# Optimization experiments

Measured on AMD Instinct MI355X. Metric: run time of the kernel, lower is better.

## Reference

```python
import jax, jax.numpy as jnp
import numpy as np

HEAD_DIM = 256
L2_EPS = 1e-12  # tf.math.l2_normalize default epsilon


def setup_inputs() -> dict:
    key = jax.random.key(0)
    ks = jax.random.split(key, 6)
    B, U = 64, 2048
    D_dec, D_enc = 1024, 512
    H, K, A = 4, HEAD_DIM, 1024
    s = 0.075  # RandomUniform(-0.075, 0.075) kernel init
    return {
        "dec_state": jax.random.normal(ks[0], (B, D_dec), jnp.float32),
        "enc_state": jax.random.normal(ks[1], (B, U, D_enc), jnp.float32),
        "phi_w": jax.random.uniform(ks[2], (H, D_dec, K), jnp.float32, -s, s),
        "phi_b": jnp.zeros((H, K), jnp.float32),
        "psi_w": jax.random.uniform(ks[3], (H, D_enc, K), jnp.float32, -s, s),
        "psi_b": jnp.zeros((H, K), jnp.float32),
        "out_w": jax.random.uniform(ks[4], (H * D_enc, A), jnp.float32, -s, s),
        "out_b": jnp.zeros((A,), jnp.float32),
    }


def reference(dec_state, enc_state, phi_w, phi_b, psi_w, psi_b, out_w, out_b):
    B = dec_state.shape[0]
    # Per-head query/key projections, all heads at once.
    phi_s = jnp.einsum("bd,hdk->bhk", dec_state, phi_w) + phi_b[None]      # (B,H,K)
    psi_h = jnp.einsum("bue,hek->bhuk", enc_state, psi_w) + psi_b[None, :, None]  # (B,H,U,K)
    scale = 1.0 / jnp.sqrt(jnp.asarray(HEAD_DIM, jnp.float32))
    energy = jnp.einsum("bhk,bhuk->bhu", phi_s, psi_h) * scale              # (B,H,U)
    attn = jax.nn.softmax(energy, axis=-1)
    # NOTE: the original attends over the RAW enc_state (not psi_h).
    ctx = jnp.einsum("bhu,bue->bhe", attn, enc_state)                        # (B,H,E)
    # tf.math.l2_normalize over last axis
    sq = jnp.sum(ctx * ctx, axis=-1, keepdims=True)
    ctx = ctx * jax.lax.rsqrt(jnp.maximum(sq, L2_EPS))
    combined = ctx.reshape(B, -1)                                            # (B, H*E) == concat over heads
    return combined @ out_w + out_b
```

## Files before the change

kernel.cpp:

```cpp
#include <hip/hip_runtime.h>
#include <math.h>

typedef float f2 __attribute__((ext_vector_type(2)));

constexpr int NB = 64;
constexpr int NU = 2048;
constexpr int ND = 1024;
constexpr int NE = 512;
constexpr int NH = 4;
constexpr int NK = 256;
constexpr int NA = 1024;
constexpr int NS = 16;
constexpr int ROWS_PER_BLOCK = NU / NS;
constexpr int ROWS_PER_WAVE  = ROWS_PER_BLOCK / 4;
constexpr float SCALE = 0.0625f;

constexpr int RSPLIT = 16;
constexpr int RCH = (NH*NE)/RSPLIT;
constexpr int BT = 8;

constexpr size_t WS_Q   = 0;
constexpr size_t WS_CTX = WS_Q + (size_t)NB*NH*NE;

__global__ __launch_bounds__(1024) void k_phi_q(
    const float* __restrict__ dec, const float* __restrict__ phi_w,
    const float* __restrict__ phi_b, const float* __restrict__ psi_w,
    float* __restrict__ q, float* __restrict__ ctxacc,
    const float* __restrict__ out_b, float* __restrict__ out)
{
  const int bi = blockIdx.x;
  const int b = bi >> 2;
  const int h = bi & 3;
  const int t = threadIdx.x;
  if (t < 512) ctxacc[(size_t)bi*512 + t] = 0.f;
  if (t < 256) out[(size_t)bi*256 + t] = out_b[(bi*256 + t) & (NA-1)];

  __shared__ float dec_lds[ND];
  __shared__ float par[4][NK];
  __shared__ float phi_lds[NK];
  dec_lds[t] = dec[(size_t)b*ND + t];
  __syncthreads();
  const int k  = t & 255;
  const int dq = t >> 8;
  const float* pw = phi_w + (size_t)h*ND*NK + (size_t)(dq*256)*NK + k;
  float s = 0.f;
  #pragma unroll 16
  for (int d = 0; d < 256; ++d) s += dec_lds[dq*256 + d] * pw[(size_t)d*NK];
  par[dq][k] = s;
  __syncthreads();
  if (t < NK)
    phi_lds[t] = par[0][t] + par[1][t] + par[2][t] + par[3][t] + phi_b[h*NK + t];
  __syncthreads();
  if (t < NE) {
    const float4* row = (const float4*)(psi_w + ((size_t)h*NE + t)*NK);
    float acc = 0.f;
    #pragma unroll 16
    for (int kk = 0; kk < NK/4; ++kk) {
      float4 v = row[kk];
      float4 p = ((const float4*)phi_lds)[kk];
      acc += v.x*p.x + v.y*p.y + v.z*p.z + v.w*p.w;
    }
    q[((size_t)b*NH + h)*NE + t] = acc;
  }
}

__global__ __launch_bounds__(256, 4) void k_flash(
    const float* __restrict__ enc, const float* __restrict__ qg,
    float* __restrict__ ctxacc)
{
  const int s = blockIdx.x;
  const int b = blockIdx.y;
  const int t = threadIdx.x;
  const int wave = t >> 6;
  const int lane = t & 63;

  f2 qv[NH][4];
  const float* qb = qg + (size_t)b*NH*NE;
  #pragma unroll
  for (int h = 0; h < NH; ++h) {
    float4 a0 = *(const float4*)(qb + h*NE + 4*lane);
    float4 a1 = *(const float4*)(qb + h*NE + 256 + 4*lane);
    qv[h][0] = f2{a0.x, a0.y}; qv[h][1] = f2{a0.z, a0.w};
    qv[h][2] = f2{a1.x, a1.y}; qv[h][3] = f2{a1.z, a1.w};
  }
  f2 acc2[NH][4];
  #pragma unroll
  for (int h = 0; h < NH; ++h)
    #pragma unroll
    for (int j = 0; j < 4; ++j) acc2[h][j] = f2{0.f, 0.f};

  const int u0 = s*ROWS_PER_BLOCK + wave*ROWS_PER_WAVE;
  const float* encb = enc + ((size_t)b*NU + u0)*NE;
  #pragma unroll 2
  for (int r = 0; r < ROWS_PER_WAVE; ++r) {
    float4 v0 = *(const float4*)(encb + (size_t)r*NE + 4*lane);
    float4 v1 = *(const float4*)(encb + (size_t)r*NE + 256 + 4*lane);
    f2 e0 = f2{v0.x, v0.y}, e1 = f2{v0.z, v0.w};
    f2 e2 = f2{v1.x, v1.y}, e3 = f2{v1.z, v1.w};
    float d[NH];
    #pragma unroll
    for (int h = 0; h < NH; ++h) {
      f2 p = e0*qv[h][0] + e1*qv[h][1] + e2*qv[h][2] + e3*qv[h][3];
      d[h] = p[0] + p[1];
    }
    #pragma unroll
    for (int off = 1; off < 64; off <<= 1) {
      #pragma unroll
      for (int h = 0; h < NH; ++h) d[h] += __shfl_xor(d[h], off);
    }
    #pragma unroll
    for (int h = 0; h < NH; ++h) {
      float pf = __expf(d[h] * SCALE);
      f2 pp = f2{pf, pf};
      acc2[h][0] += pp*e0; acc2[h][1] += pp*e1;
      acc2[h][2] += pp*e2; acc2[h][3] += pp*e3;
    }
  }
  __shared__ float acc_lds[4][NH][NE];
  #pragma unroll
  for (int h = 0; h < NH; ++h) {
    *(float4*)&acc_lds[wave][h][4*lane] =
        make_float4(acc2[h][0][0], acc2[h][0][1], acc2[h][1][0], acc2[h][1][1]);
    *(float4*)&acc_lds[wave][h][256 + 4*lane] =
        make_float4(acc2[h][2][0], acc2[h][2][1], acc2[h][3][0], acc2[h][3][1]);
  }
  __syncthreads();
  float* cb = ctxacc + (size_t)b*(NH*NE);
  #pragma unroll
  for (int h = 0; h < NH; ++h) {
    #pragma unroll
    for (int eo = 0; eo < 2; ++eo) {
      int e = t + eo*256;
      float v = acc_lds[0][h][e] + acc_lds[1][h][e] + acc_lds[2][h][e] + acc_lds[3][h][e];
      unsafeAtomicAdd(&cb[h*NE + e], v);
    }
  }
}

__global__ __launch_bounds__(256) void k_out(
    const float* __restrict__ ctxacc, const float* __restrict__ out_w,
    float* __restrict__ out)
{
  const int t = threadIdx.x;
  const int a = blockIdx.x*256 + t;
  const int b0 = blockIdx.y * BT;
  const int rc = blockIdx.z;
  const int h  = rc >> 2;
  const int e0 = (rc & 3) * RCH;

  __shared__ float rn_lds[BT];
  const int wv = t >> 6, lane = t & 63;
  {
    const int i = 2*wv + (lane >> 5);
    const int l32 = lane & 31;
    const float* row = ctxacc + (size_t)(b0+i)*(NH*NE) + (size_t)h*NE;
    float ss = 0.f;
    #pragma unroll
    for (int j = 0; j < 16; ++j) { float v = row[l32 + 32*j]; ss += v*v; }
    #pragma unroll
    for (int off = 1; off < 32; off <<= 1) ss += __shfl_xor(ss, off);
    if (l32 == 0) rn_lds[i] = rsqrtf(fmaxf(ss, 1e-12f));
  }
  __syncthreads();

  __shared__ float c_lds[RCH][BT];
  for (int g = t; g < RCH*BT; g += 256) {
    const int r = g & (RCH-1), i = g >> 7;
    c_lds[r][i] = ctxacc[(size_t)(b0+i)*(NH*NE) + (size_t)h*NE + e0 + r] * rn_lds[i];
  }
  __syncthreads();

  float accv[BT];
  #pragma unroll
  for (int i = 0; i < BT; ++i) accv[i] = 0.f;
  const float* w = out_w + ((size_t)rc*RCH)*NA + a;
  #pragma unroll 8
  for (int r = 0; r < RCH; ++r) {
    float wvv = w[(size_t)r*NA];
    float4 ca = *(const float4*)&c_lds[r][0];
    float4 cb = *(const float4*)&c_lds[r][4];
    accv[0] += ca.x*wvv; accv[1] += ca.y*wvv; accv[2] += ca.z*wvv; accv[3] += ca.w*wvv;
    accv[4] += cb.x*wvv; accv[5] += cb.y*wvv; accv[6] += cb.z*wvv; accv[7] += cb.w*wvv;
  }
  #pragma unroll
  for (int i = 0; i < BT; ++i)
    unsafeAtomicAdd(&out[(size_t)(b0+i)*NA + a], accv[i]);
}

extern "C" void kernel_launch(void* const* d_in, const int* in_sizes, int n_in,
                              void* d_out, int out_size, void* d_ws, size_t ws_size,
                              hipStream_t stream) {
  const float* dec   = (const float*)d_in[0];
  const float* enc   = (const float*)d_in[1];
  const float* phi_w = (const float*)d_in[2];
  const float* phi_b = (const float*)d_in[3];
  const float* psi_w = (const float*)d_in[4];
  const float* out_w = (const float*)d_in[6];
  const float* out_b = (const float*)d_in[7];
  float* out = (float*)d_out;
  float* ws = (float*)d_ws;
  float* q      = ws + WS_Q;
  float* ctxacc = ws + WS_CTX;

  hipLaunchKernelGGL(k_phi_q, dim3(NB*NH),                 dim3(1024), 0, stream,
                     dec, phi_w, phi_b, psi_w, q, ctxacc, out_b, out);
  hipLaunchKernelGGL(k_flash, dim3(NS, NB),                dim3(256),  0, stream,
                     enc, q, ctxacc);
  hipLaunchKernelGGL(k_out,   dim3(NA/256, NB/BT, RSPLIT), dim3(256),  0, stream,
                     ctxacc, out_w, out);
}
```

Before: 94.69 us.

## Split query projection into batched tiled GEMM kernels with split-K partials

Replaces the per-(batch, head) query projection kernel with two tiled GEMM kernels. Each weight element of phi_w and psi_w is now reused across 16 batch rows in registers, instead of being reread once per batch. The first kernel writes split-D partial sums to a new workspace buffer. The second reduces those partials, adds the bias, multiplies by a psi_w tile held in LDS, and accumulates q with atomics. This is meant to cut redundant weight traffic in the prologue, at the cost of an extra launch, a partial-sum buffer and atomic adds.

```diff
diff --git a/kernel.cpp b/kernel.cpp
--- a/kernel.cpp
+++ b/kernel.cpp
@@ -19,49 +19,114 @@
 constexpr int RCH = (NH*NE)/RSPLIT;
 constexpr int BT = 8;
 
+constexpr int DSP = 16;
+constexpr int KSP = 4;
+
 constexpr size_t WS_Q   = 0;
 constexpr size_t WS_CTX = WS_Q + (size_t)NB*NH*NE;
-
-__global__ __launch_bounds__(1024) void k_phi_q(
+constexpr size_t WS_P   = WS_CTX + (size_t)NB*NH*NE;
+
+__global__ __launch_bounds__(256) void k_phi(
     const float* __restrict__ dec, const float* __restrict__ phi_w,
-    const float* __restrict__ phi_b, const float* __restrict__ psi_w,
-    float* __restrict__ q, float* __restrict__ ctxacc,
+    float* __restrict__ P, float* __restrict__ q, float* __restrict__ ctxacc,
     const float* __restrict__ out_b, float* __restrict__ out)
 {
-  const int bi = blockIdx.x;
-  const int b = bi >> 2;
-  const int h = bi & 3;
-  const int t = threadIdx.x;
-  if (t < 512) ctxacc[(size_t)bi*512 + t] = 0.f;
-  if (t < 256) out[(size_t)bi*256 + t] = out_b[(bi*256 + t) & (NA-1)];
-
-  __shared__ float dec_lds[ND];
-  __shared__ float par[4][NK];
-  __shared__ float phi_lds[NK];
-  dec_lds[t] = dec[(size_t)b*ND + t];
-  __syncthreads();
-  const int k  = t & 255;
-  const int dq = t >> 8;
-  const float* pw = phi_w + (size_t)h*ND*NK + (size_t)(dq*256)*NK + k;
-  float s = 0.f;
-  #pragma unroll 16
-  for (int d = 0; d < 256; ++d) s += dec_lds[dq*256 + d] * pw[(size_t)d*NK];
-  par[dq][k] = s;
-  __syncthreads();
-  if (t < NK)
-    phi_lds[t] = par[0][t] + par[1][t] + par[2][t] + par[3][t] + phi_b[h*NK + t];
-  __syncthreads();
-  if (t < NE) {
-    const float4* row = (const float4*)(psi_w + ((size_t)h*NE + t)*NK);
-    float acc = 0.f;
-    #pragma unroll 16
-    for (int kk = 0; kk < NK/4; ++kk) {
-      float4 v = row[kk];
-      float4 p = ((const float4*)phi_lds)[kk];
-      acc += v.x*p.x + v.y*p.y + v.z*p.z + v.w*p.w;
-    }
-    q[((size_t)b*NH + h)*NE + t] = acc;
-  }
+  const int flat = blockIdx.x;
+  const int kc = flat & 3;
+  const int h  = (flat >> 2) & 3;
+  const int ds = flat >> 4;
+  const int t = threadIdx.x;
+
+  ctxacc[(size_t)flat*512 + t]       = 0.f;
+  ctxacc[(size_t)flat*512 + 256 + t] = 0.f;
+  q[(size_t)flat*512 + t]            = 0.f;
+  q[(size_t)flat*512 + 256 + t]      = 0.f;
+  out[(size_t)flat*256 + t] = out_b[(flat*256 + t) & (NA-1)];
+
+  const int d0 = ds*64, k0 = kc*64;
+
+  __shared__ float dec_t[64][68];
+  {
+    const int dd = t & 63, b4 = t >> 6;
+    #pragma unroll
+    for (int j = 0; j < 16; ++j)
+      dec_t[dd][b4*16 + j] = dec[(size_t)(b4*16 + j)*ND + d0 + dd];
+  }
+  __syncthreads();
+
+  const int k = t & 63, bq = t >> 6, b0 = bq*16;
+  float acc[16];
+  #pragma unroll
+  for (int i = 0; i < 16; ++i) acc[i] = 0.f;
+  const float* pw = phi_w + ((size_t)h*ND + d0)*NK + k0 + k;
+  #pragma unroll 4
+  for (int d = 0; d < 64; ++d) {
+    float w = pw[(size_t)d*NK];
+    float4 a0 = *(const float4*)&dec_t[d][b0];
+    float4 a1 = *(const float4*)&dec_t[d][b0+4];
+    float4 a2 = *(const float4*)&dec_t[d][b0+8];
+    float4 a3 = *(const float4*)&dec_t[d][b0+12];
+    acc[0]+=a0.x*w;  acc[1]+=a0.y*w;  acc[2]+=a0.z*w;  acc[3]+=a0.w*w;
+    acc[4]+=a1.x*w;  acc[5]+=a1.y*w;  acc[6]+=a1.z*w;  acc[7]+=a1.w*w;
+    acc[8]+=a2.x*w;  acc[9]+=a2.y*w;  acc[10]+=a2.z*w; acc[11]+=a2.w*w;
+    acc[12]+=a3.x*w; acc[13]+=a3.y*w; acc[14]+=a3.z*w; acc[15]+=a3.w*w;
+  }
+  #pragma unroll
+  for (int j = 0; j < 16; ++j)
+    P[(((size_t)ds*64 + b0 + j)*NH + h)*NK + k0 + k] = acc[j];
+}
+
+__global__ __launch_bounds__(256) void k_q(
+    const float* __restrict__ P, const float* __restrict__ phi_b,
+    const float* __restrict__ psi_w, float* __restrict__ q)
+{
+  const int flat = blockIdx.x;
+  const int ks = flat & 3;
+  const int ec = (flat >> 2) & 7;
+  const int h  = flat >> 5;
+  const int t = threadIdx.x;
+  const int k0 = ks*64, e0 = ec*64;
+
+  __shared__ float phi_red[64][68];
+  __shared__ float psi_lds[64][65];
+
+  {
+    const int kk = t & 63, e4 = t >> 6;
+    #pragma unroll
+    for (int j = 0; j < 16; ++j)
+      psi_lds[e4*16 + j][kk] =
+          psi_w[((size_t)h*NE + e0 + e4*16 + j)*NK + k0 + kk];
+  }
+  #pragma unroll
+  for (int g = t; g < 64*64; g += 256) {
+    const int b = g >> 6, kl = g & 63;
+    float s = 0.f;
+    #pragma unroll
+    for (int ds = 0; ds < DSP; ++ds)
+      s += P[(((size_t)ds*64 + b)*NH + h)*NK + k0 + kl];
+    phi_red[kl][b] = s + phi_b[h*NK + k0 + kl];
+  }
+  __syncthreads();
+
+  const int e = t & 63, bq = t >> 6, b0 = bq*16;
+  float acc[16];
+  #pragma unroll
+  for (int i = 0; i < 16; ++i) acc[i] = 0.f;
+  #pragma unroll 4
+  for (int kl = 0; kl < 64; ++kl) {
+    float w = psi_lds[e][kl];
+    float4 a0 = *(const float4*)&phi_red[kl][b0];
+    float4 a1 = *(const float4*)&phi_red[kl][b0+4];
+    float4 a2 = *(const float4*)&phi_red[kl][b0+8];
+    float4 a3 = *(const float4*)&phi_red[kl][b0+12];
+    acc[0]+=a0.x*w;  acc[1]+=a0.y*w;  acc[2]+=a0.z*w;  acc[3]+=a0.w*w;
+    acc[4]+=a1.x*w;  acc[5]+=a1.y*w;  acc[6]+=a1.z*w;  acc[7]+=a1.w*w;
+    acc[8]+=a2.x*w;  acc[9]+=a2.y*w;  acc[10]+=a2.z*w; acc[11]+=a2.w*w;
+    acc[12]+=a3.x*w; acc[13]+=a3.y*w; acc[14]+=a3.z*w; acc[15]+=a3.w*w;
+  }
+  #pragma unroll
+  for (int j = 0; j < 16; ++j)
+    unsafeAtomicAdd(&q[((size_t)(b0 + j)*NH + h)*NE + e0 + e], acc[j]);
 }
 
 __global__ __launch_bounds__(256, 4) void k_flash(
@@ -201,11 +266,14 @@
   float* ws = (float*)d_ws;
   float* q      = ws + WS_Q;
   float* ctxacc = ws + WS_CTX;
-
-  hipLaunchKernelGGL(k_phi_q, dim3(NB*NH),                 dim3(1024), 0, stream,
-                     dec, phi_w, phi_b, psi_w, q, ctxacc, out_b, out);
-  hipLaunchKernelGGL(k_flash, dim3(NS, NB),                dim3(256),  0, stream,
+  float* P      = ws + WS_P;
+
+  hipLaunchKernelGGL(k_phi,   dim3(NH*4*DSP),              dim3(256), 0, stream,
+                     dec, phi_w, P, q, ctxacc, out_b, out);
+  hipLaunchKernelGGL(k_q,     dim3(NH*8*KSP),              dim3(256), 0, stream,
+                     P, phi_b, psi_w, q);
+  hipLaunchKernelGGL(k_flash, dim3(NS, NB),                dim3(256), 0, stream,
                      enc, q, ctxacc);
-  hipLaunchKernelGGL(k_out,   dim3(NA/256, NB/BT, RSPLIT), dim3(256),  0, stream,
+  hipLaunchKernelGGL(k_out,   dim3(NA/256, NB/BT, RSPLIT), dim3(256), 0, stream,
                      ctxacc, out_w, out);
 }
```

New measurement: 90.13 us. 1.05x faster.
